# Kernel tuning notes

Measured on AMD Instinct MI355X. Metric: run time of the kernel, lower is better.

## Reference

```python
import jax, jax.numpy as jnp
import numpy as np

BATCH, T, N = 8, 2048, 512


def setup_inputs() -> dict:
    key = jax.random.key(0)
    ks = jax.random.split(key, 8)
    scale = 1.0 / np.sqrt(2.0 * (N + N) / 2.0) / np.sqrt(2.0)  # GlorotNormal / sqrt(2)
    u = jax.random.normal(ks[0], (BATCH, T, N), dtype=jnp.float32)
    C_re = jax.random.normal(ks[1], (N, N), dtype=jnp.float32) * scale
    C_im = jax.random.normal(ks[2], (N, N), dtype=jnp.float32) * scale
    B_re = jax.random.normal(ks[3], (N, N), dtype=jnp.float32) * scale
    B_im = jax.random.normal(ks[4], (N, N), dtype=jnp.float32) * scale
    D = jax.random.normal(ks[5], (N,), dtype=jnp.float32)
    # nu drawn from the numerically-stable end of [log(-log rmax), log(-log rmin)]
    nu = jax.random.uniform(ks[6], (N,), minval=-4.6, maxval=-3.7, dtype=jnp.float32)
    theta = jax.random.uniform(ks[7], (N,), minval=0.0, maxval=3.14 / 10, dtype=jnp.float32)
    # gamma initialized as sqrt(1 - |lambda|^2), lambda = exp(-exp(nu) + i*theta)
    gamma = jnp.sqrt(1.0 - jnp.exp(-2.0 * jnp.exp(nu)))
    return {"u": u, "C_re": C_re, "C_im": C_im, "B_re": B_re, "B_im": B_im,
            "D": D, "nu": nu, "theta": theta, "gamma": gamma}


def reference(u, C_re, C_im, B_re, B_im, D, nu, theta, gamma):
    # log_lambda = -exp(nu) + i*theta  (the TF code names this `lambda_`)
    log_lam = (-jnp.exp(nu)).astype(jnp.complex64) + 1j * theta.astype(jnp.complex64)  # (n,)
    t = jnp.arange(u.shape[1], dtype=jnp.float32).astype(jnp.complex64)[:, None]       # (T,1)
    lam_pow = jnp.exp(log_lam[None, :] * t)    # (T,n) == diag(Lambda^t)
    lam_minpow = jnp.exp(-log_lam[None, :] * t)  # (T,n) == diag(Lambda^-t)
    Bm = (B_re + 1j * B_im).astype(jnp.complex64)  # (n,n)
    Cm = (C_re + 1j * C_im).astype(jnp.complex64)  # (n,n)
    # new_u = (gamma * u) @ B   (complex)
    new_u = (gamma * u).astype(jnp.complex64) @ Bm  # (b,t,n)
    # diag einsums in the original are elementwise multiplies
    x = jnp.cumsum(new_u * lam_minpow[None], axis=1) * lam_pow[None]  # (b,t,n)
    y = jnp.real(x @ Cm) + D * u
    return y
```

## Files before the change

### kernel.cpp

```cpp
#include <hip/hip_runtime.h>
#include <hip/hip_bf16.h>
#include <math.h>
#include <stdint.h>

#define BATCH 8
#define T_LEN 2048
#define NDIM 512
#define M_ROWS (BATCH * T_LEN)
#define CHUNK 32
#define NCHUNK (T_LEN / CHUNK)


typedef __attribute__((ext_vector_type(8))) short bf16x8;
typedef __attribute__((ext_vector_type(4))) float floatx4;

#define VMWAIT(n) asm volatile("s_waitcnt vmcnt(" #n ")" ::: "memory")

__device__ __forceinline__ unsigned short f2bf(float f) {
    union { float f; unsigned u; } v; v.f = f;
    unsigned r = v.u + 0x7fff + ((v.u >> 16) & 1);
    return (unsigned short)(r >> 16);
}
__device__ __forceinline__ float bf2f(unsigned short h) {
    union { unsigned u; float f; } v; v.u = ((unsigned)h) << 16;
    return v.f;
}
__device__ __forceinline__ float bf2f_lo(unsigned u) {
    union { unsigned u; float f; } v; v.u = u << 16; return v.f;
}
__device__ __forceinline__ float bf2f_hi(unsigned u) {
    union { unsigned u; float f; } v; v.u = u & 0xffff0000u; return v.f;
}

__device__ __forceinline__ void gld_lds16(const unsigned short* g, unsigned short* l) {
    __builtin_amdgcn_global_load_lds(
        (const __attribute__((address_space(1))) unsigned int*)(uintptr_t)g,
        (__attribute__((address_space(3))) unsigned int*)(uintptr_t)l,
        16, 0, 0);
}

__global__ __launch_bounds__(256) void k_prep(
    const float* __restrict__ u,
    const float* __restrict__ Bre, const float* __restrict__ Bim,
    const float* __restrict__ Cre, const float* __restrict__ Cim,
    const float* __restrict__ gamma,
    unsigned short* __restrict__ ubf,
    unsigned short* __restrict__ BT, unsigned short* __restrict__ CT)
{
    __shared__ unsigned short tile[32][33];
    const int blk = blockIdx.x;
    if (blk < 4096) {
        size_t i = ((size_t)blk * 256 + threadIdx.x) * 8;
        float4 a = *(const float4*)&u[i];
        float4 b = *(const float4*)&u[i + 4];
        ushort4 p0, p1;
        p0.x = f2bf(a.x); p0.y = f2bf(a.y); p0.z = f2bf(a.z); p0.w = f2bf(a.w);
        p1.x = f2bf(b.x); p1.y = f2bf(b.y); p1.z = f2bf(b.z); p1.w = f2bf(b.w);
        *(ushort4*)&ubf[i] = p0;
        *(ushort4*)&ubf[i + 4] = p1;
        return;
    }
    const int p = blk - 4096;
    const int z = p >> 8;
    const int rem = p & 255;
    const int n0 = (rem & 15) * 32, k0 = (rem >> 4) * 32;
    const float* __restrict__ src = (z == 0) ? Bre : (z == 1) ? Bim : (z == 2) ? Cre : Cim;
    const int tx = threadIdx.x & 31, ty = threadIdx.x >> 5;

#pragma unroll
    for (int j = 0; j < 4; ++j) {
        int k = k0 + ty + j * 8;
        float s = (z < 2) ? gamma[k] : (z == 3 ? -1.f : 1.f);
        tile[ty + j * 8][tx] = f2bf(s * src[(size_t)k * NDIM + n0 + tx]);
    }
    __syncthreads();
#pragma unroll
    for (int j = 0; j < 4; ++j) {
        int n = n0 + ty + j * 8;
        unsigned short v = tile[tx][ty + j * 8];
        if (z == 0) {
            int row = ((n >> 6) << 7) + (n & 63);
            BT[(size_t)row * 512 + k0 + tx] = v;
        } else if (z == 1) {
            int row = ((n >> 6) << 7) + 64 + (n & 63);
            BT[(size_t)row * 512 + k0 + tx] = v;
        } else if (z == 2) {
            int k = k0 + tx;
            int col = ((k >> 6) << 7) + (k & 63);
            CT[(size_t)n * 1024 + col] = v;
        } else {
            int k = k0 + tx;
            int col = ((k >> 6) << 7) + 64 + (k & 63);
            CT[(size_t)n * 1024 + col] = v;
        }
    }
}

__global__ __launch_bounds__(512) void k_gemm_in(
    const unsigned short* __restrict__ A,
    const unsigned short* __restrict__ BT,
    const float* __restrict__ nu, const float* __restrict__ theta,
    unsigned short* __restrict__ X,
    float* __restrict__ carry)
{
    __shared__ unsigned short smem[65536];

    const int tid = threadIdx.x;
    const int w = tid >> 6, l = tid & 63;
    const int bm = blockIdx.x * 256;
    const int bn = blockIdx.y * 256;
    const int wm = (w & 1) * 128, wn = (w >> 1) * 64;
    const int lm = l & 15, lq = l >> 4;
    const int sr = tid >> 3;
    const int scw = ((tid & 7) ^ (sr & 7)) * 8;
    const int scl = (tid & 7) * 8;
    const int rsw = (lm & 7) << 3;

    floatx4 acc[8][4];
#pragma unroll
    for (int i = 0; i < 8; ++i)
#pragma unroll
        for (int j = 0; j < 4; ++j) acc[i][j] = (floatx4)0.f;

    auto SPAIR = [&](int buf, int t, int pair) {
        unsigned short* as = &smem[buf * 32768];
        unsigned short* bs = as + 16384;
        const int k0 = t * 64;
        if (pair == 0) {
            gld_lds16(&BT[(size_t)(bn + 0 * 64 + sr) * 512 + k0 + scw], &bs[(0 * 64 + sr) * 64 + scl]);
            gld_lds16(&BT[(size_t)(bn + 1 * 64 + sr) * 512 + k0 + scw], &bs[(1 * 64 + sr) * 64 + scl]);
        } else if (pair == 1) {
            gld_lds16(&BT[(size_t)(bn + 2 * 64 + sr) * 512 + k0 + scw], &bs[(2 * 64 + sr) * 64 + scl]);
            gld_lds16(&BT[(size_t)(bn + 3 * 64 + sr) * 512 + k0 + scw], &bs[(3 * 64 + sr) * 64 + scl]);
        } else if (pair == 2) {
            gld_lds16(&A[(size_t)(bm + 0 * 64 + sr) * 512 + k0 + scw], &as[(0 * 64 + sr) * 64 + scl]);
            gld_lds16(&A[(size_t)(bm + 2 * 64 + sr) * 512 + k0 + scw], &as[(2 * 64 + sr) * 64 + scl]);
        } else {
            gld_lds16(&A[(size_t)(bm + 1 * 64 + sr) * 512 + k0 + scw], &as[(1 * 64 + sr) * 64 + scl]);
            gld_lds16(&A[(size_t)(bm + 3 * 64 + sr) * 512 + k0 + scw], &as[(3 * 64 + sr) * 64 + scl]);
        }
    };

    auto PHASE = [&](int buf, int qa, int qb, int stt, int pair) {
        const unsigned short* as = &smem[buf * 32768];
        const unsigned short* bs = as + 16384;
        bf16x8 af[4][2], bfr[2][2];
#pragma unroll
        for (int i4 = 0; i4 < 4; ++i4)
#pragma unroll
            for (int ks = 0; ks < 2; ++ks)
                af[i4][ks] = *(const bf16x8*)&as[(wm + (qa * 4 + i4) * 16 + lm) * 64 + ((ks * 32 + lq * 8) ^ rsw)];
#pragma unroll
        for (int j2 = 0; j2 < 2; ++j2)
#pragma unroll
            for (int ks = 0; ks < 2; ++ks)
                bfr[j2][ks] = *(const bf16x8*)&bs[(wn + (qb * 2 + j2) * 16 + lm) * 64 + ((ks * 32 + lq * 8) ^ rsw)];
        if (pair >= 0) SPAIR(buf ^ 1, stt, pair);
        __builtin_amdgcn_s_setprio(1);
#pragma unroll
        for (int i4 = 0; i4 < 4; ++i4)
#pragma unroll
            for (int j2 = 0; j2 < 2; ++j2)
#pragma unroll
                for (int ks = 0; ks < 2; ++ks)
                    acc[qa * 4 + i4][qb * 2 + j2] = __builtin_amdgcn_mfma_f32_16x16x32_bf16(
                        af[i4][ks], bfr[j2][ks], acc[qa * 4 + i4][qb * 2 + j2], 0, 0, 0);
        __builtin_amdgcn_s_setprio(0);
    };

    SPAIR(0, 0, 0); SPAIR(0, 0, 1); SPAIR(0, 0, 2); SPAIR(0, 0, 3);
    VMWAIT(2);
    __builtin_amdgcn_s_barrier();
    __builtin_amdgcn_sched_barrier(0);

#pragma unroll
    for (int t = 0; t < 8; ++t) {
        const int ct = t & 1;
        const bool st = (t < 7);
        PHASE(ct, 0, 0, t + 1, st ? 0 : -1);
        PHASE(ct, 0, 1, t + 1, st ? 1 : -1);
        if (st) { VMWAIT(4); } else { VMWAIT(0); }
        __builtin_amdgcn_s_barrier();
        __builtin_amdgcn_sched_barrier(0);
        PHASE(ct, 1, 0, t + 1, st ? 2 : -1);
        PHASE(ct, 1, 1, t + 1, st ? 3 : -1);
        if (st) {
            VMWAIT(2);
            __builtin_amdgcn_s_barrier();
            __builtin_amdgcn_sched_barrier(0);
        }
    }

    __syncthreads();
#pragma unroll
    for (int i = 0; i < 8; ++i)
#pragma unroll
        for (int j = 0; j < 4; ++j) {
            int lcol = wn + j * 16 + lm;
#pragma unroll
            for (int r = 0; r < 4; ++r) {
                int lrow = wm + i * 16 + lq * 4 + r;
                unsigned short v = f2bf(acc[i][j][r]);
                smem[lrow * 256 + lcol] = v;
                X[(size_t)(bm + lrow) * 1024 + bn + lcol] = v;
            }
        }
    __syncthreads();
#pragma unroll
    for (int q = 0; q < 2; ++q) {
        const int s = tid + q * 512;
        const int chunk = s >> 7;
        const int ch = s & 127;
        const int n = (bn >> 1) + ch;
        const int gl = ch >> 6, cc = ch & 63;
        const int recol = gl * 128 + cc;
        const float rr = __expf(-__expf(nu[n]));
        const float lre = rr * __cosf(theta[n]);
        const float lim = rr * __sinf(theta[n]);
        const unsigned short* base = &smem[chunk * 32 * 256 + recol];
        float xre = 0.f, xim = 0.f;
#pragma unroll 8
        for (int t = 0; t < 32; ++t) {
            float ure = bf2f(base[t * 256]);
            float uim = bf2f(base[t * 256 + 64]);
            float a = lre * xre - lim * xim + ure;
            float b = lre * xim + lim * xre + uim;
            xre = a; xim = b;
        }
        const int bb = bm >> 11;
        const int cg = ((bm & 2047) >> 5) + chunk;
        size_t ci = ((size_t)bb * NCHUNK + cg) * NDIM + n;
        *(float2*)&carry[ci * 2] = make_float2(xre, xim);
    }
}

__global__ __launch_bounds__(256) void k_scan_apply(
    unsigned short* __restrict__ X,
    const float* __restrict__ nu, const float* __restrict__ theta,
    const float* __restrict__ carry)
{
    const int t2 = threadIdx.x;
    const int n0 = 2 * t2;
    const int b = blockIdx.x >> 6, c = blockIdx.x & 63;
    const float ex0 = __expf(nu[n0]), ex1 = __expf(nu[n0 + 1]);
    const float r0 = __expf(-ex0), r1 = __expf(-ex1);
    const float lre0 = r0 * __cosf(theta[n0]),     lim0 = r0 * __sinf(theta[n0]);
    const float lre1 = r1 * __cosf(theta[n0 + 1]), lim1 = r1 * __sinf(theta[n0 + 1]);
    const float rc0 = expf(-ex0 * (float)CHUNK), rc1 = expf(-ex1 * (float)CHUNK);
    const float th0 = theta[n0] * (float)CHUNK,  th1 = theta[n0 + 1] * (float)CHUNK;
    const float A0 = rc0 * cosf(th0), B0 = rc0 * sinf(th0);
    const float A1 = rc1 * cosf(th1), B1 = rc1 * sinf(th1);

    float xre0 = 0.f, xim0 = 0.f, xre1 = 0.f, xim1 = 0.f;
    for (int cc = 0; cc < c; ++cc) {
        size_t idx = ((size_t)b * NCHUNK + cc) * NDIM + n0;
        float4 cv = *(const float4*)&carry[idx * 2];
        float a0 = A0 * xre0 - B0 * xim0 + cv.x;
        float b0 = A0 * xim0 + B0 * xre0 + cv.y;
        float a1 = A1 * xre1 - B1 * xim1 + cv.z;
        float b1 = A1 * xim1 + B1 * xre1 + cv.w;
        xre0 = a0; xim0 = b0; xre1 = a1; xim1 = b1;
    }

    const int recol = ((n0 >> 6) << 7) + (n0 & 63);
    size_t m = (size_t)b * T_LEN + (size_t)c * CHUNK;
#pragma unroll 8
    for (int t = 0; t < CHUNK; ++t, ++m) {
        unsigned re = *(const unsigned*)&X[m * 1024 + recol];
        unsigned im = *(const unsigned*)&X[m * 1024 + recol + 64];
        float u0 = bf2f_lo(re), u1 = bf2f_hi(re);
        float v0 = bf2f_lo(im), v1 = bf2f_hi(im);
        float a0 = lre0 * xre0 - lim0 * xim0 + u0;
        float b0 = lre0 * xim0 + lim0 * xre0 + v0;
        float a1 = lre1 * xre1 - lim1 * xim1 + u1;
        float b1 = lre1 * xim1 + lim1 * xre1 + v1;
        xre0 = a0; xim0 = b0; xre1 = a1; xim1 = b1;
        unsigned pr = (unsigned)f2bf(xre0) | ((unsigned)f2bf(xre1) << 16);
        unsigned pim = (unsigned)f2bf(xim0) | ((unsigned)f2bf(xim1) << 16);
        *(unsigned*)&X[m * 1024 + recol] = pr;
        *(unsigned*)&X[m * 1024 + recol + 64] = pim;
    }
}

__global__ __launch_bounds__(512) void k_gemm_out(
    const unsigned short* __restrict__ Xbf,
    const unsigned short* __restrict__ CT,
    const float* __restrict__ D,
    const unsigned short* __restrict__ Ubf,
    float* __restrict__ Y)
{
    __shared__ unsigned short smem[73728];

    const int tid = threadIdx.x;
    const int w = tid >> 6, l = tid & 63;
    const int bm = blockIdx.x * 256;
    const int bn = blockIdx.y * 128;
    const int wm = (w & 3) * 64, wn = (w >> 2) * 64;
    const int lm = l & 15, lq = l >> 4;
    const int sr = tid >> 3;
    const int scw = ((tid & 7) ^ (sr & 7)) * 8;
    const int scl = (tid & 7) * 8;
    const int rsw = (lm & 7) << 3;

    floatx4 acc[4][4];
#pragma unroll
    for (int i = 0; i < 4; ++i)
#pragma unroll
        for (int j = 0; j < 4; ++j) acc[i][j] = (floatx4)0.f;

    auto SHALF = [&](int buf, int t, int half) {
        unsigned short* as = &smem[buf * 24576];
        unsigned short* bs = as + 16384;
        const int k0 = t * 64;
        if (half == 0) {
            gld_lds16(&Xbf[(size_t)(bm + 0 * 64 + sr) * 1024 + k0 + scw], &as[(0 * 64 + sr) * 64 + scl]);
            gld_lds16(&Xbf[(size_t)(bm + 1 * 64 + sr) * 1024 + k0 + scw], &as[(1 * 64 + sr) * 64 + scl]);
            gld_lds16(&CT[(size_t)(bn + 0 * 64 + sr) * 1024 + k0 + scw],  &bs[(0 * 64 + sr) * 64 + scl]);
        } else {
            gld_lds16(&Xbf[(size_t)(bm + 2 * 64 + sr) * 1024 + k0 + scw], &as[(2 * 64 + sr) * 64 + scl]);
            gld_lds16(&Xbf[(size_t)(bm + 3 * 64 + sr) * 1024 + k0 + scw], &as[(3 * 64 + sr) * 64 + scl]);
            gld_lds16(&CT[(size_t)(bn + 1 * 64 + sr) * 1024 + k0 + scw],  &bs[(1 * 64 + sr) * 64 + scl]);
        }
    };

    auto PHASE = [&](int buf, int p, int sbuf, int stt, int half) {
        const unsigned short* as = &smem[buf * 24576];
        const unsigned short* bs = as + 16384;
        bf16x8 af[4][2], bfr[2][2];
#pragma unroll
        for (int i = 0; i < 4; ++i)
#pragma unroll
            for (int ks = 0; ks < 2; ++ks)
                af[i][ks] = *(const bf16x8*)&as[(wm + i * 16 + lm) * 64 + ((ks * 32 + lq * 8) ^ rsw)];
#pragma unroll
        for (int j2 = 0; j2 < 2; ++j2)
#pragma unroll
            for (int ks = 0; ks < 2; ++ks)
                bfr[j2][ks] = *(const bf16x8*)&bs[(wn + (p * 2 + j2) * 16 + lm) * 64 + ((ks * 32 + lq * 8) ^ rsw)];
        if (half >= 0) SHALF(sbuf, stt, half);
        __builtin_amdgcn_s_setprio(1);
#pragma unroll
        for (int i = 0; i < 4; ++i)
#pragma unroll
            for (int j2 = 0; j2 < 2; ++j2)
#pragma unroll
                for (int ks = 0; ks < 2; ++ks)
                    acc[i][p * 2 + j2] = __builtin_amdgcn_mfma_f32_16x16x32_bf16(
                        af[i][ks], bfr[j2][ks], acc[i][p * 2 + j2], 0, 0, 0);
        __builtin_amdgcn_s_setprio(0);
    };

    SHALF(0, 0, 0); SHALF(0, 0, 1);
    SHALF(1, 1, 0); SHALF(1, 1, 1);
    VMWAIT(6);
    __builtin_amdgcn_s_barrier();
    __builtin_amdgcn_sched_barrier(0);

#pragma unroll
    for (int t = 0; t < 16; ++t) {
        const int ct = t % 3;
        const int sb = (t + 2) % 3;
        const bool st = (t < 14);
        PHASE(ct, 0, sb, t + 2, st ? 0 : -1);
        PHASE(ct, 1, sb, t + 2, st ? 1 : -1);
        if (t < 15) {
            if (st) { VMWAIT(6); } else { VMWAIT(0); }
            __builtin_amdgcn_s_barrier();
            __builtin_amdgcn_sched_barrier(0);
        }
    }

#pragma unroll
    for (int i = 0; i < 4; ++i)
#pragma unroll
        for (int j = 0; j < 4; ++j) {
            int col = bn + wn + j * 16 + lm;
            float dv = D[col];
#pragma unroll
            for (int r = 0; r < 4; ++r) {
                int row = bm + wm + i * 16 + lq * 4 + r;
                size_t off = (size_t)row * NDIM + col;
                Y[off] = acc[i][j][r] + dv * bf2f(Ubf[off]);
            }
        }
}

extern "C" void kernel_launch(void* const* d_in, const int* in_sizes, int n_in,
                              void* d_out, int out_size, void* d_ws, size_t ws_size,
                              hipStream_t stream)
{
    const float* u     = (const float*)d_in[0];
    const float* C_re  = (const float*)d_in[1];
    const float* C_im  = (const float*)d_in[2];
    const float* B_re  = (const float*)d_in[3];
    const float* B_im  = (const float*)d_in[4];
    const float* D     = (const float*)d_in[5];
    const float* nu    = (const float*)d_in[6];
    const float* theta = (const float*)d_in[7];
    const float* gamma = (const float*)d_in[8];
    float* y = (float*)d_out;

    unsigned short* X   = (unsigned short*)d_ws;
    unsigned short* ubf = X + (size_t)M_ROWS * 1024;
    unsigned short* BT  = ubf + (size_t)M_ROWS * 512;
    unsigned short* CT  = BT + (size_t)1024 * 512;
    float* carry = (float*)(CT + (size_t)512 * 1024);

    k_prep<<<4096 + 1024, 256, 0, stream>>>(u, B_re, B_im, C_re, C_im, gamma, ubf, BT, CT);
    k_gemm_in<<<dim3(M_ROWS / 256, 4), 512, 0, stream>>>(ubf, BT, nu, theta, X, carry);
    k_scan_apply<<<BATCH * NCHUNK, 256, 0, stream>>>(X, nu, theta, carry);
    k_gemm_out<<<dim3(M_ROWS / 256, 4), 512, 0, stream>>>(X, CT, D, ubf, y);
}
```

Before: 166.7 us.

## Fuse chunked scan application into output GEMM via LDS-resident tile

Merges the scan-apply kernel and the output GEMM into one kernel. Each block owns one 32-step chunk of one batch. It rebuilds the chunk's starting state from the per-chunk carries, runs the recurrence, and writes the bf16 states into a swizzled LDS tile. It then multiplies that tile against the full C^T, which is streamed through double-buffered LDS. This removes the global write-back and re-read of the 32 MB state buffer and one kernel launch. In exchange the GEMM tiles become thin (32x512), each block re-reads all of C^T, there is a barrier at every K step, and the large LDS footprint limits occupancy.

```diff
diff --git a/kernel.cpp b/kernel.cpp
--- a/kernel.cpp
+++ b/kernel.cpp
@@ -234,153 +234,121 @@
     }
 }
 
-__global__ __launch_bounds__(256) void k_scan_apply(
-    unsigned short* __restrict__ X,
+__global__ __launch_bounds__(512) void k_scan_gemm(
+    const unsigned short* __restrict__ X,
+    const unsigned short* __restrict__ CT,
     const float* __restrict__ nu, const float* __restrict__ theta,
-    const float* __restrict__ carry)
-{
-    const int t2 = threadIdx.x;
-    const int n0 = 2 * t2;
-    const int b = blockIdx.x >> 6, c = blockIdx.x & 63;
-    const float ex0 = __expf(nu[n0]), ex1 = __expf(nu[n0 + 1]);
-    const float r0 = __expf(-ex0), r1 = __expf(-ex1);
-    const float lre0 = r0 * __cosf(theta[n0]),     lim0 = r0 * __sinf(theta[n0]);
-    const float lre1 = r1 * __cosf(theta[n0 + 1]), lim1 = r1 * __sinf(theta[n0 + 1]);
-    const float rc0 = expf(-ex0 * (float)CHUNK), rc1 = expf(-ex1 * (float)CHUNK);
-    const float th0 = theta[n0] * (float)CHUNK,  th1 = theta[n0 + 1] * (float)CHUNK;
-    const float A0 = rc0 * cosf(th0), B0 = rc0 * sinf(th0);
-    const float A1 = rc1 * cosf(th1), B1 = rc1 * sinf(th1);
-
-    float xre0 = 0.f, xim0 = 0.f, xre1 = 0.f, xim1 = 0.f;
-    for (int cc = 0; cc < c; ++cc) {
-        size_t idx = ((size_t)b * NCHUNK + cc) * NDIM + n0;
-        float4 cv = *(const float4*)&carry[idx * 2];
-        float a0 = A0 * xre0 - B0 * xim0 + cv.x;
-        float b0 = A0 * xim0 + B0 * xre0 + cv.y;
-        float a1 = A1 * xre1 - B1 * xim1 + cv.z;
-        float b1 = A1 * xim1 + B1 * xre1 + cv.w;
-        xre0 = a0; xim0 = b0; xre1 = a1; xim1 = b1;
-    }
-
-    const int recol = ((n0 >> 6) << 7) + (n0 & 63);
-    size_t m = (size_t)b * T_LEN + (size_t)c * CHUNK;
-#pragma unroll 8
-    for (int t = 0; t < CHUNK; ++t, ++m) {
-        unsigned re = *(const unsigned*)&X[m * 1024 + recol];
-        unsigned im = *(const unsigned*)&X[m * 1024 + recol + 64];
-        float u0 = bf2f_lo(re), u1 = bf2f_hi(re);
-        float v0 = bf2f_lo(im), v1 = bf2f_hi(im);
-        float a0 = lre0 * xre0 - lim0 * xim0 + u0;
-        float b0 = lre0 * xim0 + lim0 * xre0 + v0;
-        float a1 = lre1 * xre1 - lim1 * xim1 + u1;
-        float b1 = lre1 * xim1 + lim1 * xre1 + v1;
-        xre0 = a0; xim0 = b0; xre1 = a1; xim1 = b1;
-        unsigned pr = (unsigned)f2bf(xre0) | ((unsigned)f2bf(xre1) << 16);
-        unsigned pim = (unsigned)f2bf(xim0) | ((unsigned)f2bf(xim1) << 16);
-        *(unsigned*)&X[m * 1024 + recol] = pr;
-        *(unsigned*)&X[m * 1024 + recol + 64] = pim;
-    }
-}
-
-__global__ __launch_bounds__(512) void k_gemm_out(
-    const unsigned short* __restrict__ Xbf,
-    const unsigned short* __restrict__ CT,
+    const float* __restrict__ carry,
     const float* __restrict__ D,
     const unsigned short* __restrict__ Ubf,
     float* __restrict__ Y)
 {
-    __shared__ unsigned short smem[73728];
+    __shared__ unsigned short Asm[32 * 1024];
+    __shared__ unsigned short Bsm[2][512 * 32];
 
     const int tid = threadIdx.x;
+    const int c = blockIdx.x, b = blockIdx.y;
+    const int m0 = b * T_LEN + c * CHUNK;
+
+    const int brow4 = tid >> 2;
+    const int bslot = tid & 3;
+    auto SB = [&](int buf, int t) {
+        const int k0 = t * 32;
+#pragma unroll
+        for (int o = 0; o < 4; ++o) {
+            int row = o * 128 + brow4;
+            gld_lds16(&CT[(size_t)row * 1024 + k0 + ((bslot ^ (row & 3)) * 8)],
+                      &Bsm[buf][row * 32 + bslot * 8]);
+        }
+    };
+
+    SB(0, 0);
+    SB(1, 1);
+
+    const int n = tid;
+    const float ex = __expf(nu[n]);
+    const float r0 = __expf(-ex);
+    const float lre = r0 * __cosf(theta[n]);
+    const float lim = r0 * __sinf(theta[n]);
+    const float rc = expf(-ex * (float)CHUNK);
+    const float th = theta[n] * (float)CHUNK;
+    const float A0 = rc * cosf(th), B0 = rc * sinf(th);
+    float xre = 0.f, xim = 0.f;
+    for (int cc = 0; cc < c; ++cc) {
+        float2 cv = *(const float2*)&carry[(((size_t)b * NCHUNK + cc) * NDIM + n) * 2];
+        float a  = A0 * xre - B0 * xim + cv.x;
+        float b2 = A0 * xim + B0 * xre + cv.y;
+        xre = a; xim = b2;
+    }
+
+    const int recol = ((n >> 6) << 7) + (n & 63);
+#pragma unroll 8
+    for (int t = 0; t < 32; ++t) {
+        size_t m = (size_t)(m0 + t) * 1024;
+        float ure = bf2f(X[m + recol]);
+        float uim = bf2f(X[m + recol + 64]);
+        float a  = lre * xre - lim * xim + ure;
+        float b2 = lre * xim + lim * xre + uim;
+        xre = a; xim = b2;
+        const int sw = (t & 7) << 3;
+        Asm[t * 1024 + (recol ^ sw)] = f2bf(xre);
+        Asm[t * 1024 + ((recol + 64) ^ sw)] = f2bf(xim);
+    }
+
+    __syncthreads();
+
     const int w = tid >> 6, l = tid & 63;
-    const int bm = blockIdx.x * 256;
-    const int bn = blockIdx.y * 128;
-    const int wm = (w & 3) * 64, wn = (w >> 2) * 64;
+    const int wn = w * 64;
     const int lm = l & 15, lq = l >> 4;
-    const int sr = tid >> 3;
-    const int scw = ((tid & 7) ^ (sr & 7)) * 8;
-    const int scl = (tid & 7) * 8;
-    const int rsw = (lm & 7) << 3;
-
-    floatx4 acc[4][4];
-#pragma unroll
-    for (int i = 0; i < 4; ++i)
-#pragma unroll
-        for (int j = 0; j < 4; ++j) acc[i][j] = (floatx4)0.f;
-
-    auto SHALF = [&](int buf, int t, int half) {
-        unsigned short* as = &smem[buf * 24576];
-        unsigned short* bs = as + 16384;
-        const int k0 = t * 64;
-        if (half == 0) {
-            gld_lds16(&Xbf[(size_t)(bm + 0 * 64 + sr) * 1024 + k0 + scw], &as[(0 * 64 + sr) * 64 + scl]);
-            gld_lds16(&Xbf[(size_t)(bm + 1 * 64 + sr) * 1024 + k0 + scw], &as[(1 * 64 + sr) * 64 + scl]);
-            gld_lds16(&CT[(size_t)(bn + 0 * 64 + sr) * 1024 + k0 + scw],  &bs[(0 * 64 + sr) * 64 + scl]);
-        } else {
-            gld_lds16(&Xbf[(size_t)(bm + 2 * 64 + sr) * 1024 + k0 + scw], &as[(2 * 64 + sr) * 64 + scl]);
-            gld_lds16(&Xbf[(size_t)(bm + 3 * 64 + sr) * 1024 + k0 + scw], &as[(3 * 64 + sr) * 64 + scl]);
-            gld_lds16(&CT[(size_t)(bn + 1 * 64 + sr) * 1024 + k0 + scw],  &bs[(1 * 64 + sr) * 64 + scl]);
-        }
-    };
-
-    auto PHASE = [&](int buf, int p, int sbuf, int stt, int half) {
-        const unsigned short* as = &smem[buf * 24576];
-        const unsigned short* bs = as + 16384;
-        bf16x8 af[4][2], bfr[2][2];
-#pragma unroll
-        for (int i = 0; i < 4; ++i)
-#pragma unroll
-            for (int ks = 0; ks < 2; ++ks)
-                af[i][ks] = *(const bf16x8*)&as[(wm + i * 16 + lm) * 64 + ((ks * 32 + lq * 8) ^ rsw)];
-#pragma unroll
-        for (int j2 = 0; j2 < 2; ++j2)
-#pragma unroll
-            for (int ks = 0; ks < 2; ++ks)
-                bfr[j2][ks] = *(const bf16x8*)&bs[(wn + (p * 2 + j2) * 16 + lm) * 64 + ((ks * 32 + lq * 8) ^ rsw)];
-        if (half >= 0) SHALF(sbuf, stt, half);
+    const int asw = (lm & 7) << 3;
+    const int bsw = (lm & 3) << 3;
+
+    floatx4 acc[2][4];
+#pragma unroll
+    for (int mi = 0; mi < 2; ++mi)
+#pragma unroll
+        for (int j = 0; j < 4; ++j) acc[mi][j] = (floatx4)0.f;
+
+    auto COMPUTE = [&](int buf, int t) {
+        const int k0 = t * 32;
+        bf16x8 af[2], bfr[4];
+#pragma unroll
+        for (int mi = 0; mi < 2; ++mi)
+            af[mi] = *(const bf16x8*)&Asm[(mi * 16 + lm) * 1024 + ((k0 + lq * 8) ^ asw)];
+#pragma unroll
+        for (int j = 0; j < 4; ++j)
+            bfr[j] = *(const bf16x8*)&Bsm[buf][(wn + j * 16 + lm) * 32 + ((lq * 8) ^ bsw)];
         __builtin_amdgcn_s_setprio(1);
 #pragma unroll
-        for (int i = 0; i < 4; ++i)
-#pragma unroll
-            for (int j2 = 0; j2 < 2; ++j2)
-#pragma unroll
-                for (int ks = 0; ks < 2; ++ks)
-                    acc[i][p * 2 + j2] = __builtin_amdgcn_mfma_f32_16x16x32_bf16(
-                        af[i][ks], bfr[j2][ks], acc[i][p * 2 + j2], 0, 0, 0);
+        for (int mi = 0; mi < 2; ++mi)
+#pragma unroll
+            for (int j = 0; j < 4; ++j)
+                acc[mi][j] = __builtin_amdgcn_mfma_f32_16x16x32_bf16(af[mi], bfr[j], acc[mi][j], 0, 0, 0);
         __builtin_amdgcn_s_setprio(0);
     };
 
-    SHALF(0, 0, 0); SHALF(0, 0, 1);
-    SHALF(1, 1, 0); SHALF(1, 1, 1);
-    VMWAIT(6);
-    __builtin_amdgcn_s_barrier();
-    __builtin_amdgcn_sched_barrier(0);
-
-#pragma unroll
-    for (int t = 0; t < 16; ++t) {
-        const int ct = t % 3;
-        const int sb = (t + 2) % 3;
-        const bool st = (t < 14);
-        PHASE(ct, 0, sb, t + 2, st ? 0 : -1);
-        PHASE(ct, 1, sb, t + 2, st ? 1 : -1);
-        if (t < 15) {
-            if (st) { VMWAIT(6); } else { VMWAIT(0); }
-            __builtin_amdgcn_s_barrier();
-            __builtin_amdgcn_sched_barrier(0);
-        }
-    }
-
-#pragma unroll
-    for (int i = 0; i < 4; ++i)
+#pragma unroll 4
+    for (int t = 0; t < 32; ++t) {
+        if (t < 31) { VMWAIT(4); } else { VMWAIT(0); }
+        __builtin_amdgcn_s_barrier();
+        __builtin_amdgcn_sched_barrier(0);
+        COMPUTE(t & 1, t);
+        __builtin_amdgcn_s_barrier();
+        __builtin_amdgcn_sched_barrier(0);
+        if (t < 30) SB(t & 1, t + 2);
+    }
+
+#pragma unroll
+    for (int mi = 0; mi < 2; ++mi)
 #pragma unroll
         for (int j = 0; j < 4; ++j) {
-            int col = bn + wn + j * 16 + lm;
+            int col = wn + j * 16 + lm;
             float dv = D[col];
 #pragma unroll
             for (int r = 0; r < 4; ++r) {
-                int row = bm + wm + i * 16 + lq * 4 + r;
-                size_t off = (size_t)row * NDIM + col;
-                Y[off] = acc[i][j][r] + dv * bf2f(Ubf[off]);
+                int row = mi * 16 + lq * 4 + r;
+                size_t off = (size_t)(m0 + row) * NDIM + col;
+                Y[off] = acc[mi][j][r] + dv * bf2f(Ubf[off]);
             }
         }
 }
@@ -408,6 +376,5 @@
 
     k_prep<<<4096 + 1024, 256, 0, stream>>>(u, B_re, B_im, C_re, C_im, gamma, ubf, BT, CT);
     k_gemm_in<<<dim3(M_ROWS / 256, 4), 512, 0, stream>>>(ubf, BT, nu, theta, X, carry);
-    k_scan_apply<<<BATCH * NCHUNK, 256, 0, stream>>>(X, nu, theta, carry);
-    k_gemm_out<<<dim3(M_ROWS / 256, 4), 512, 0, stream>>>(X, CT, D, ubf, y);
-}
+    k_scan_gemm<<<dim3(NCHUNK, BATCH), 512, 0, stream>>>(X, CT, nu, theta, carry, D, ubf, y);
+}
```

New measurement: 196.5 us. 1.18x slower.

## Fuse chunk scan into input GEMM using inter-block flag synchronization

Applied to the files above, without the earlier changes.

Removes the separate scan-apply kernel. Each input-GEMM block publishes its per-chunk carries with atomic stores and raises a flag. It then spins on the flags of earlier blocks in the same batch sequence, computes its starting state from prior carries, and writes the fully scanned X directly from LDS. This avoids writing X once and then re-reading and rewriting it in another kernel, plus one launch. The cost is a dependency on earlier blocks being resident or already finished; if they are not co-scheduled, blocks may spin-wait or deadlock.

```diff
diff --git a/kernel.cpp b/kernel.cpp
--- a/kernel.cpp
+++ b/kernel.cpp
@@ -16,6 +16,8 @@
 
 #define VMWAIT(n) asm volatile("s_waitcnt vmcnt(" #n ")" ::: "memory")
 
+union F2U { float2 f2; unsigned long long u; };
+
 __device__ __forceinline__ unsigned short f2bf(float f) {
     union { float f; unsigned u; } v; v.f = f;
     unsigned r = v.u + 0x7fff + ((v.u >> 16) & 1);
@@ -24,12 +26,6 @@
 __device__ __forceinline__ float bf2f(unsigned short h) {
     union { unsigned u; float f; } v; v.u = ((unsigned)h) << 16;
     return v.f;
-}
-__device__ __forceinline__ float bf2f_lo(unsigned u) {
-    union { unsigned u; float f; } v; v.u = u << 16; return v.f;
-}
-__device__ __forceinline__ float bf2f_hi(unsigned u) {
-    union { unsigned u; float f; } v; v.u = u & 0xffff0000u; return v.f;
 }
 
 __device__ __forceinline__ void gld_lds16(const unsigned short* g, unsigned short* l) {
@@ -45,11 +41,13 @@
     const float* __restrict__ Cre, const float* __restrict__ Cim,
     const float* __restrict__ gamma,
     unsigned short* __restrict__ ubf,
-    unsigned short* __restrict__ BT, unsigned short* __restrict__ CT)
+    unsigned short* __restrict__ BT, unsigned short* __restrict__ CT,
+    int* __restrict__ flags)
 {
     __shared__ unsigned short tile[32][33];
     const int blk = blockIdx.x;
     if (blk < 4096) {
+        if (blk == 0) flags[threadIdx.x] = 0;
         size_t i = ((size_t)blk * 256 + threadIdx.x) * 8;
         float4 a = *(const float4*)&u[i];
         float4 b = *(const float4*)&u[i + 4];
@@ -101,7 +99,8 @@
     const unsigned short* __restrict__ BT,
     const float* __restrict__ nu, const float* __restrict__ theta,
     unsigned short* __restrict__ X,
-    float* __restrict__ carry)
+    float* __restrict__ carry,
+    int* __restrict__ flags)
 {
     __shared__ unsigned short smem[65536];
 
@@ -200,85 +199,112 @@
 #pragma unroll
             for (int r = 0; r < 4; ++r) {
                 int lrow = wm + i * 16 + lq * 4 + r;
-                unsigned short v = f2bf(acc[i][j][r]);
-                smem[lrow * 256 + lcol] = v;
-                X[(size_t)(bm + lrow) * 1024 + bn + lcol] = v;
+                smem[lrow * 256 + lcol] = f2bf(acc[i][j][r]);
             }
         }
     __syncthreads();
-#pragma unroll
-    for (int q = 0; q < 2; ++q) {
-        const int s = tid + q * 512;
-        const int chunk = s >> 7;
-        const int ch = s & 127;
+
+    const int bb = bm >> 11;
+    const int cg0 = (bm & 2047) >> 5;
+    {
+#pragma unroll
+        for (int q = 0; q < 2; ++q) {
+            const int s = tid + q * 512;
+            const int chunk = s >> 7;
+            const int ch = s & 127;
+            const int n = (bn >> 1) + ch;
+            const int gl = ch >> 6, cc2 = ch & 63;
+            const int rc_ = gl * 128 + cc2;
+            const float rr = __expf(-__expf(nu[n]));
+            const float lre = rr * __cosf(theta[n]);
+            const float lim = rr * __sinf(theta[n]);
+            const unsigned short* base = &smem[chunk * 32 * 256 + rc_];
+            float xre = 0.f, xim = 0.f;
+#pragma unroll 8
+            for (int t = 0; t < 32; ++t) {
+                float ure = bf2f(base[t * 256]);
+                float uim = bf2f(base[t * 256 + 64]);
+                float a = lre * xre - lim * xim + ure;
+                float b = lre * xim + lim * xre + uim;
+                xre = a; xim = b;
+            }
+            F2U cv; cv.f2 = make_float2(xre, xim);
+            size_t ci = ((size_t)bb * NCHUNK + (cg0 + chunk)) * NDIM + n;
+            __hip_atomic_store((unsigned long long*)&carry[ci * 2], cv.u,
+                               __ATOMIC_RELAXED, __HIP_MEMORY_SCOPE_AGENT);
+        }
+    }
+    __threadfence();
+    __syncthreads();
+    if (tid == 0)
+        __hip_atomic_store(&flags[blockIdx.y * 64 + blockIdx.x], 1,
+                           __ATOMIC_RELEASE, __HIP_MEMORY_SCOPE_AGENT);
+
+    const int p8 = blockIdx.x & 7;
+    if (p8) {
+        if (tid < p8) {
+            int f = blockIdx.y * 64 + (blockIdx.x - 1 - tid);
+            while (__hip_atomic_load(&flags[f], __ATOMIC_ACQUIRE,
+                                     __HIP_MEMORY_SCOPE_AGENT) == 0)
+                __builtin_amdgcn_s_sleep(1);
+        }
+        __syncthreads();
+    }
+
+    {
+        const int chunk = tid >> 7;
+        const int ch = tid & 127;
         const int n = (bn >> 1) + ch;
-        const int gl = ch >> 6, cc = ch & 63;
-        const int recol = gl * 128 + cc;
-        const float rr = __expf(-__expf(nu[n]));
+        const int gl = ch >> 6, cc2 = ch & 63;
+        const int rc_ = gl * 128 + cc2;
+        const float ex = __expf(nu[n]);
+        const float rr = __expf(-ex);
         const float lre = rr * __cosf(theta[n]);
         const float lim = rr * __sinf(theta[n]);
-        const unsigned short* base = &smem[chunk * 32 * 256 + recol];
+        const float rc = expf(-ex * (float)CHUNK);
+        const float th = theta[n] * (float)CHUNK;
+        const float A0 = rc * cosf(th), B0 = rc * sinf(th);
+
         float xre = 0.f, xim = 0.f;
+        const int cgA = cg0 + chunk;
+        for (int cc = 0; cc < cgA; ++cc) {
+            F2U cv;
+            cv.u = __hip_atomic_load(
+                (unsigned long long*)&carry[(((size_t)bb * NCHUNK + cc) * NDIM + n) * 2],
+                __ATOMIC_RELAXED, __HIP_MEMORY_SCOPE_AGENT);
+            float a = A0 * xre - B0 * xim + cv.f2.x;
+            float b = A0 * xim + B0 * xre + cv.f2.y;
+            xre = a; xim = b;
+        }
+        float yre = xre, yim = xim;
+        for (int cc = cgA; cc < cgA + 4; ++cc) {
+            F2U cv;
+            cv.u = __hip_atomic_load(
+                (unsigned long long*)&carry[(((size_t)bb * NCHUNK + cc) * NDIM + n) * 2],
+                __ATOMIC_RELAXED, __HIP_MEMORY_SCOPE_AGENT);
+            float a = A0 * yre - B0 * yim + cv.f2.x;
+            float b = A0 * yim + B0 * yre + cv.f2.y;
+            yre = a; yim = b;
+        }
+
+#pragma unroll
+        for (int half = 0; half < 2; ++half) {
+            const int ck = chunk + half * 4;
+            float sre = half ? yre : xre;
+            float sim = half ? yim : xim;
+            const unsigned short* base = &smem[ck * 32 * 256 + rc_];
+            unsigned short* xg = &X[(size_t)(bm + ck * 32) * 1024 + bn + rc_];
 #pragma unroll 8
-        for (int t = 0; t < 32; ++t) {
-            float ure = bf2f(base[t * 256]);
-            float uim = bf2f(base[t * 256 + 64]);
-            float a = lre * xre - lim * xim + ure;
-            float b = lre * xim + lim * xre + uim;
-            xre = a; xim = b;
-        }
-        const int bb = bm >> 11;
-        const int cg = ((bm & 2047) >> 5) + chunk;
-        size_t ci = ((size_t)bb * NCHUNK + cg) * NDIM + n;
-        *(float2*)&carry[ci * 2] = make_float2(xre, xim);
-    }
-}
-
-__global__ __launch_bounds__(256) void k_scan_apply(
-    unsigned short* __restrict__ X,
-    const float* __restrict__ nu, const float* __restrict__ theta,
-    const float* __restrict__ carry)
-{
-    const int t2 = threadIdx.x;
-    const int n0 = 2 * t2;
-    const int b = blockIdx.x >> 6, c = blockIdx.x & 63;
-    const float ex0 = __expf(nu[n0]), ex1 = __expf(nu[n0 + 1]);
-    const float r0 = __expf(-ex0), r1 = __expf(-ex1);
-    const float lre0 = r0 * __cosf(theta[n0]),     lim0 = r0 * __sinf(theta[n0]);
-    const float lre1 = r1 * __cosf(theta[n0 + 1]), lim1 = r1 * __sinf(theta[n0 + 1]);
-    const float rc0 = expf(-ex0 * (float)CHUNK), rc1 = expf(-ex1 * (float)CHUNK);
-    const float th0 = theta[n0] * (float)CHUNK,  th1 = theta[n0 + 1] * (float)CHUNK;
-    const float A0 = rc0 * cosf(th0), B0 = rc0 * sinf(th0);
-    const float A1 = rc1 * cosf(th1), B1 = rc1 * sinf(th1);
-
-    float xre0 = 0.f, xim0 = 0.f, xre1 = 0.f, xim1 = 0.f;
-    for (int cc = 0; cc < c; ++cc) {
-        size_t idx = ((size_t)b * NCHUNK + cc) * NDIM + n0;
-        float4 cv = *(const float4*)&carry[idx * 2];
-        float a0 = A0 * xre0 - B0 * xim0 + cv.x;
-        float b0 = A0 * xim0 + B0 * xre0 + cv.y;
-        float a1 = A1 * xre1 - B1 * xim1 + cv.z;
-        float b1 = A1 * xim1 + B1 * xre1 + cv.w;
-        xre0 = a0; xim0 = b0; xre1 = a1; xim1 = b1;
-    }
-
-    const int recol = ((n0 >> 6) << 7) + (n0 & 63);
-    size_t m = (size_t)b * T_LEN + (size_t)c * CHUNK;
-#pragma unroll 8
-    for (int t = 0; t < CHUNK; ++t, ++m) {
-        unsigned re = *(const unsigned*)&X[m * 1024 + recol];
-        unsigned im = *(const unsigned*)&X[m * 1024 + recol + 64];
-        float u0 = bf2f_lo(re), u1 = bf2f_hi(re);
-        float v0 = bf2f_lo(im), v1 = bf2f_hi(im);
-        float a0 = lre0 * xre0 - lim0 * xim0 + u0;
-        float b0 = lre0 * xim0 + lim0 * xre0 + v0;
-        float a1 = lre1 * xre1 - lim1 * xim1 + u1;
-        float b1 = lre1 * xim1 + lim1 * xre1 + v1;
-        xre0 = a0; xim0 = b0; xre1 = a1; xim1 = b1;
-        unsigned pr = (unsigned)f2bf(xre0) | ((unsigned)f2bf(xre1) << 16);
-        unsigned pim = (unsigned)f2bf(xim0) | ((unsigned)f2bf(xim1) << 16);
-        *(unsigned*)&X[m * 1024 + recol] = pr;
-        *(unsigned*)&X[m * 1024 + recol + 64] = pim;
+            for (int t = 0; t < 32; ++t) {
+                float ure = bf2f(base[t * 256]);
+                float uim = bf2f(base[t * 256 + 64]);
+                float a = lre * sre - lim * sim + ure;
+                float b = lre * sim + lim * sre + uim;
+                sre = a; sim = b;
+                xg[(size_t)t * 1024] = f2bf(sre);
+                xg[(size_t)t * 1024 + 64] = f2bf(sim);
+            }
+        }
     }
 }
 
@@ -405,9 +431,9 @@
     unsigned short* BT  = ubf + (size_t)M_ROWS * 512;
     unsigned short* CT  = BT + (size_t)1024 * 512;
     float* carry = (float*)(CT + (size_t)512 * 1024);
-
-    k_prep<<<4096 + 1024, 256, 0, stream>>>(u, B_re, B_im, C_re, C_im, gamma, ubf, BT, CT);
-    k_gemm_in<<<dim3(M_ROWS / 256, 4), 512, 0, stream>>>(ubf, BT, nu, theta, X, carry);
-    k_scan_apply<<<BATCH * NCHUNK, 256, 0, stream>>>(X, nu, theta, carry);
+    int* flags = (int*)(carry + (size_t)BATCH * NCHUNK * NDIM * 2);
+
+    k_prep<<<4096 + 1024, 256, 0, stream>>>(u, B_re, B_im, C_re, C_im, gamma, ubf, BT, CT, flags);
+    k_gemm_in<<<dim3(M_ROWS / 256, 4), 512, 0, stream>>>(ubf, BT, nu, theta, X, carry, flags);
     k_gemm_out<<<dim3(M_ROWS / 256, 4), 512, 0, stream>>>(X, CT, D, ubf, y);
 }
```

Result: slower. 187.7 us (+12.6%).
